# Kernel tuning notes

Hardware: AMD Instinct MI355X
Metric: run time of the kernel (lower is better)

Reference implementation:

```python
import jax, jax.numpy as jnp
import numpy as np

L, H, C = 2, 2, 128            # conv layers, heads, out_channels
N, E, B = 10000, 100000, 64    # nodes, edges, graphs
F_NODE, F_EDGE, FC = 92, 50, 512
HC, C3 = H * C, 3 * C


def _ln(x, g, b, eps=1e-5):
    m = x.mean(-1, keepdims=True)
    v = jnp.var(x, axis=-1, keepdims=True)
    return (x - m) * jax.lax.rsqrt(v + eps) * g + b


def setup_inputs() -> dict:
    key = jax.random.key(0)
    ks = jax.random.split(key, 20)
    r = lambda i, shape, s=0.05: jax.random.normal(ks[i], shape, jnp.float32) * s
    d = {}
    d["x"] = jax.random.normal(ks[0], (N, F_NODE), jnp.float32)
    d["edge_attr"] = jax.random.normal(ks[1], (E, F_EDGE), jnp.float32)
    d["pge"] = jax.random.normal(ks[2], (B, 32), jnp.float32)
    d["cse"] = jax.random.normal(ks[3], (B, 7), jnp.float32)
    d["edge_index"] = jax.random.randint(ks[4], (2, E), 0, N, jnp.int32)
    d["batch"] = jnp.sort(jax.random.randint(ks[5], (N,), 0, B, jnp.int32))
    d["atom_W"] = r(6, (F_NODE, C)); d["atom_b"] = jnp.zeros(C)
    d["edge_W"] = r(7, (F_EDGE, C)); d["edge_b"] = jnp.zeros(C)
    d["Wq"] = r(8, (L, C, HC)); d["bq"] = jnp.zeros((L, HC))
    d["Wk"] = r(9, (L, C, HC)); d["bk"] = jnp.zeros((L, HC))
    d["Wv"] = r(10, (L, C, HC)); d["bv"] = jnp.zeros((L, HC))
    d["We"] = r(11, (L, C, HC))
    d["Wmu"] = r(12, (L, C3, C3)); d["bmu"] = jnp.zeros((L, C3))
    d["Wm"] = r(13, (L, C3, C)); d["bm"] = jnp.zeros((L, C))
    d["ln_m_g"] = jnp.ones((L, C)); d["ln_m_b"] = jnp.zeros((L, C))
    d["ln_a_g"] = jnp.ones((L, C3)); d["ln_a_b"] = jnp.zeros((L, C3))
    d["Wc"] = r(14, (L, HC, C)); d["bc"] = jnp.zeros((L, C))
    d["bn_g"] = jnp.ones((L, C)); d["bn_b"] = jnp.zeros((L, C))
    d["Wskip"] = r(15, (L, C, C)); d["bskip"] = jnp.zeros((L, C))
    d["fc_W"] = r(16, (C + 32 + 7, FC)); d["fc_b"] = jnp.zeros(FC)
    d["out_W"] = r(17, (FC, 1)); d["out_b"] = jnp.zeros(1)
    return d


def reference(x, edge_attr, pge, cse, edge_index, batch, atom_W, atom_b,
              edge_W, edge_b, Wq, bq, Wk, bk, Wv, bv, We, Wmu, bmu, Wm, bm,
              ln_m_g, ln_m_b, ln_a_g, ln_a_b, Wc, bc, bn_g, bn_b, Wskip,
              bskip, fc_W, fc_b, out_W, out_b):
    src, dst = edge_index[0], edge_index[1]  # j = source, i = target
    nf = x @ atom_W + atom_b                 # [N, C]
    ef = edge_attr @ edge_W + edge_b         # [E, C]
    scale = 1.0 / np.sqrt(C3).astype(np.float32)
    for i in range(L):
        q = (nf @ Wq[i] + bq[i]).reshape(N, H, C)
        k = (nf @ Wk[i] + bk[i]).reshape(N, H, C)
        v = (nf @ Wv[i] + bv[i]).reshape(N, H, C)
        ea = (ef @ We[i]).reshape(E, H, C)
        qi = q[dst]
        qcat = jnp.concatenate([qi, qi, qi], -1)                 # [E,H,3C]
        kcat = jnp.concatenate([k[dst], k[src], ea], -1)         # [E,H,3C]
        alpha = qcat * kcat * scale
        gate = jax.nn.sigmoid(_ln(alpha, ln_a_g[i], ln_a_b[i]))
        m = jnp.concatenate([v[dst], v[src], ea], -1)            # [E,H,3C]
        m = (jnp.einsum('ehf,fg->ehg', m, Wmu[i]) + bmu[i]) * gate
        m = jnp.einsum('ehf,fc->ehc', m, Wm[i]) + bm[i]          # [E,H,C]
        m = _ln(m, ln_m_g[i], ln_m_b[i])
        agg = jax.ops.segment_sum(m, dst, num_segments=N)        # scatter-add
        o = agg.reshape(N, HC) @ Wc[i] + bc[i]                   # lin_concate
        mu = o.mean(0); var = jnp.var(o, axis=0)                 # BN (batch stats)
        o = (o - mu) * jax.lax.rsqrt(var + 1e-5) * bn_g[i] + bn_b[i]
        o = jax.nn.silu(o)
        nf = o + nf @ Wskip[i] + bskip[i]                        # root skip
    sums = jax.ops.segment_sum(nf, batch, num_segments=B)
    cnt = jax.ops.segment_sum(jnp.ones((N, 1), nf.dtype), batch, num_segments=B)
    pooled = sums / jnp.maximum(cnt, 1.0)                        # global_mean_pool
    feats = jnp.concatenate([pooled, pge, cse], 1)               # [B, C+39]
    h = jax.nn.silu(feats @ fc_W + fc_b)
    return h @ out_W + out_b                                     # [B, 1]
```

## Files before the change

### kernel.cpp

```cpp
#include <hip/hip_runtime.h>
#include <math.h>

#define N_NODES 10000
#define N_EDGES 100000
#define N_GRAPH 64
#define CDIM 128
#define HCDIM 256
#define C3DIM 384

typedef unsigned short u16;
typedef __attribute__((ext_vector_type(8))) short bf16x8;
typedef __attribute__((ext_vector_type(4))) float f32x4;

__device__ __forceinline__ u16 f2bf(float f) {
  union { float f; unsigned int u; } x; x.f = f;
  unsigned int u = x.u + 0x7fffu + ((x.u >> 16) & 1u);
  return (u16)(u >> 16);
}
__device__ __forceinline__ float bf2f(u16 h) {
  union { unsigned int u; float f; } x; x.u = ((unsigned int)h) << 16;
  return x.f;
}

template<int OUT_BF16, int DO_STATS>
__global__ __launch_bounds__(256) void mfma_gemm_kernel(
    const u16* __restrict__ Ab, const u16* __restrict__ WT,
    const float* __restrict__ bias, void* __restrict__ Y,
    u16* __restrict__ Ymirror, float* __restrict__ cs, float* __restrict__ cs2,
    int M, int K, int N) {
  const int tid = threadIdx.x;
  const int w = tid >> 6, l = tid & 63;
  const int lq = l >> 4, ln = l & 15;
  const int bm = blockIdx.y * 128, bn = blockIdx.x * 64;
  int ra = bm + w * 32 + ln;      if (ra > M - 1) ra = M - 1;
  int rb = bm + w * 32 + 16 + ln; if (rb > M - 1) rb = M - 1;
  f32x4 acc[2][4];
#pragma unroll
  for (int g = 0; g < 2; ++g)
#pragma unroll
    for (int nt = 0; nt < 4; ++nt) acc[g][nt] = {0.f, 0.f, 0.f, 0.f};
  for (int k0 = 0; k0 < K; k0 += 32) {
    bf16x8 a0 = *(const bf16x8*)&Ab[(size_t)ra * K + k0 + lq * 8];
    bf16x8 a1 = *(const bf16x8*)&Ab[(size_t)rb * K + k0 + lq * 8];
#pragma unroll
    for (int nt = 0; nt < 4; ++nt) {
      bf16x8 b = *(const bf16x8*)&WT[(size_t)(bn + nt * 16 + ln) * K + k0 + lq * 8];
      acc[0][nt] = __builtin_amdgcn_mfma_f32_16x16x32_bf16(a0, b, acc[0][nt], 0, 0, 0);
      acc[1][nt] = __builtin_amdgcn_mfma_f32_16x16x32_bf16(a1, b, acc[1][nt], 0, 0, 0);
    }
  }
#pragma unroll
  for (int g = 0; g < 2; ++g) {
    int rowbase = bm + w * 32 + g * 16 + lq * 4;
#pragma unroll
    for (int nt = 0; nt < 4; ++nt) {
      int gn = bn + nt * 16 + ln;
      float bv = bias ? bias[gn] : 0.f;
#pragma unroll
      for (int r = 0; r < 4; ++r) {
        int gm = rowbase + r;
        if (gm < M) {
          float val = acc[g][nt][r] + bv;
          if (OUT_BF16) ((u16*)Y)[(size_t)gm * N + gn] = f2bf(val);
          else          ((float*)Y)[(size_t)gm * N + gn] = val;
          if (Ymirror)  Ymirror[(size_t)gm * N + gn] = f2bf(val);
        }
      }
    }
  }
  if (DO_STATS) {
#pragma unroll
    for (int nt = 0; nt < 4; ++nt) {
      int gn = bn + nt * 16 + ln;
      float bv = bias ? bias[gn] : 0.f;
      float s = 0.f, s2 = 0.f;
#pragma unroll
      for (int g = 0; g < 2; ++g) {
        int rowbase = bm + w * 32 + g * 16 + lq * 4;
#pragma unroll
        for (int r = 0; r < 4; ++r) {
          if (rowbase + r < M) {
            float v = acc[g][nt][r] + bv;
            s += v; s2 += v * v;
          }
        }
      }
      s += __shfl_xor(s, 16); s2 += __shfl_xor(s2, 16);
      s += __shfl_xor(s, 32); s2 += __shfl_xor(s2, 32);
      if (lq == 0) { atomicAdd(&cs[gn], s); atomicAdd(&cs2[gn], s2); }
    }
  }
}

__global__ void pack_init_kernel(
    const float* __restrict__ x, const float* __restrict__ ea,
    const float* __restrict__ atom_W, const float* __restrict__ edge_W,
    u16* __restrict__ xpad, u16* __restrict__ epad,
    u16* __restrict__ atomWT, u16* __restrict__ WeT2) {
  int z = blockIdx.y;
  int idx0 = blockIdx.x * 256 + threadIdx.x;
  const int stride = 256 * 256;
  if (z == 0) {
    for (int idx = idx0; idx < N_NODES * 96; idx += stride) {
      int n = idx / 96, k = idx - n * 96;
      xpad[idx] = (k < 92) ? f2bf(x[(size_t)n * 92 + k]) : (u16)0;
    }
  } else if (z == 1) {
    for (int idx = idx0; idx < N_EDGES * 64; idx += stride) {
      int e = idx >> 6, k = idx & 63;
      epad[idx] = (k < 50) ? f2bf(ea[(size_t)e * 50 + k]) : (u16)0;
    }
  } else if (z == 2) {
    if (idx0 < 128 * 96) { int n = idx0 / 96, k = idx0 - n * 96;
      atomWT[idx0] = (k < 92) ? f2bf(atom_W[(size_t)k * 128 + n]) : (u16)0; }
  } else {
    if (idx0 < 128 * 64) { int n = idx0 >> 6, k = idx0 & 63;
      WeT2[idx0] = (k < 50) ? f2bf(edge_W[(size_t)k * 128 + n]) : (u16)0; }
  }
}

__global__ __launch_bounds__(256) void compose_kernel(
    const float* __restrict__ Wv, const float* __restrict__ We,
    const float* __restrict__ Wmu, u16* __restrict__ WallT,
    u16* __restrict__ WcT) {
  const int z = blockIdx.z;
  const float* Ap; const float* Bp;
  u16* Cp; int colbase;
  if (z < 4) {
    int part = z >> 1, h = z & 1;
    Ap = Wv + h * 128; Bp = Wmu + part * 128 * 384;
    Cp = WallT; colbase = 512 + part * 768 + h * 384;
  } else {
    int h = z - 4;
    Ap = We + h * 128; Bp = Wmu + 256 * 384;
    Cp = WcT; colbase = 256 + h * 384;
  }
  __shared__ float As[16][68];
  __shared__ float Bs[16][65];
  const int tid = threadIdx.x;
  const int bm = blockIdx.y * 64, bn = blockIdx.x * 64;
  const int tx = tid & 15, ty = tid >> 4;
  float acc[4][4] = {};
  for (int k0 = 0; k0 < 128; k0 += 16) {
#pragma unroll
    for (int i = 0; i < 4; ++i) {
      int l = tid + i * 256;
      int kk = l & 15, m = l >> 4;
      As[kk][m] = Ap[(size_t)(bm + m) * 256 + k0 + kk];
    }
#pragma unroll
    for (int i = 0; i < 4; ++i) {
      int l = tid + i * 256;
      int n = l & 63, kk = l >> 6;
      Bs[kk][n] = Bp[(size_t)(k0 + kk) * 384 + bn + n];
    }
    __syncthreads();
#pragma unroll
    for (int kk = 0; kk < 16; ++kk) {
      float a[4], b[4];
#pragma unroll
      for (int i = 0; i < 4; ++i) a[i] = As[kk][ty * 4 + i];
#pragma unroll
      for (int j = 0; j < 4; ++j) b[j] = Bs[kk][tx * 4 + j];
#pragma unroll
      for (int i = 0; i < 4; ++i)
#pragma unroll
        for (int j = 0; j < 4; ++j) acc[i][j] += a[i] * b[j];
    }
    __syncthreads();
  }
#pragma unroll
  for (int i = 0; i < 4; ++i) {
    int gk = bm + ty * 4 + i;
#pragma unroll
    for (int j = 0; j < 4; ++j) {
      int gcol = colbase + bn + tx * 4 + j;
      Cp[(size_t)gcol * 128 + gk] = f2bf(acc[i][j]);
    }
  }
}

__global__ void pack_all_kernel(
    const float* __restrict__ Wq, const float* __restrict__ Wk,
    const float* __restrict__ Wc, const float* __restrict__ Wsk,
    const float* __restrict__ Wm_l, const float* __restrict__ bmu,
    const float* __restrict__ bv_l, const float* __restrict__ Wmu,
    const float* __restrict__ bq_l, const float* __restrict__ bk_l,
    const float* __restrict__ We_l,
    u16* __restrict__ WallT, u16* __restrict__ WcTw, u16* __restrict__ WskT,
    u16* __restrict__ WmTb, float* __restrict__ cbv, float* __restrict__ ball,
    float* __restrict__ agg, float* __restrict__ cs, float* __restrict__ cs2,
    u16* __restrict__ WcT) {
  int z = blockIdx.y;
  int idx = blockIdx.x * 256 + threadIdx.x;
  if (z == 0) {
    if (idx < 32768) { int col = idx >> 7, kk = idx & 127;
      WallT[(size_t)col * 128 + kk] = f2bf(Wq[(size_t)kk * 256 + col]); }
  } else if (z == 1) {
    if (idx < 32768) { int col = idx >> 7, kk = idx & 127;
      WallT[(size_t)(256 + col) * 128 + kk] = f2bf(Wk[(size_t)kk * 256 + col]); }
  } else if (z == 2) {
    if (idx < 32768) { int col = idx >> 8, kk = idx & 255;
      WcTw[(size_t)col * 256 + kk] = f2bf(Wc[(size_t)kk * 128 + col]); }
  } else if (z == 3) {
    if (idx < 16384) { int col = idx >> 7, kk = idx & 127;
      WskT[(size_t)col * 128 + kk] = f2bf(Wsk[(size_t)kk * 128 + col]); }
  } else if (z == 4) {
    if (idx < 49152) { int col = idx / 384, kk = idx - col * 384;
      WmTb[idx] = f2bf(Wm_l[(size_t)kk * 128 + col]); }
  } else if (z == 5) {
    if (idx < 768) {
      int h2 = idx / 384, g = idx - h2 * 384;
      float s = bmu[g];
      for (int d = 0; d < 128; ++d)
        s += bv_l[h2 * 128 + d] * (Wmu[(size_t)d * 384 + g] + Wmu[(size_t)(128 + d) * 384 + g]);
      cbv[idx] = s;
    }
  } else if (z == 6) {
    if (idx < 2048) {
      float v = 0.f;
      if (idx < 256) v = bq_l[idx];
      else if (idx < 512) v = bk_l[idx - 256];
      ball[idx] = v;
    }
  } else if (z == 7) {
    for (int p = idx; p < N_NODES * HCDIM; p += 192 * 256) agg[p] = 0.f;
    if (idx < 128) { cs[idx] = 0.f; cs2[idx] = 0.f; }
  } else {
    if (idx < 32768) { int col = idx >> 7, kk = idx & 127;
      WcT[(size_t)col * 128 + kk] = f2bf(We_l[(size_t)kk * 256 + col]); }
  }
}

__global__ void pack_bf16_kernel(const float* __restrict__ A, u16* __restrict__ B, int n) {
  int idx = blockIdx.x * blockDim.x + threadIdx.x;
  if (idx < n) B[idx] = f2bf(A[idx]);
}

__global__ __launch_bounds__(256, 3) void edge_kernel(
    const u16* __restrict__ qkp, const u16* __restrict__ efb,
    const int* __restrict__ ei, const u16* __restrict__ WcT,
    const float* __restrict__ cbv,
    const float* __restrict__ lag, const float* __restrict__ lab,
    const u16* __restrict__ WmT, const float* __restrict__ bm_l,
    const float* __restrict__ lmg, const float* __restrict__ lmb,
    float* __restrict__ agg, int E) {
  __shared__ __align__(16) u16 C1[16 * 1032];
  __shared__ __align__(16) u16 A2p[12 * 512];
  __shared__ int did16[16];
  float* C2 = (float*)A2p;
  const int tid = threadIdx.x;
  const int e0 = blockIdx.x * 16;
  const int w = tid >> 6, l = tid & 63;
  const int lq = l >> 4, ln = l & 15;
  const float scale = 0.051031036307982884f;

  if (tid < 16) did16[tid] = ei[E + e0 + tid];

  const int r = tid >> 4, lx = tid & 15;
  const int hA = r >> 3, eA = r & 7;

  bf16x8 qv[2], kdv[2], ksv[2], pdv[2][3], psv[2][3];
#pragma unroll
  for (int s = 0; s < 2; ++s) {
    int edge = e0 + s * 8 + eA;
    int dstn = ei[E + edge], srcn = ei[edge];
    const u16* db = qkp + (size_t)dstn * 2048;
    const u16* sb = qkp + (size_t)srcn * 2048;
    qv[s]  = *(const bf16x8*)&db[hA * 128 + lx * 8];
    kdv[s] = *(const bf16x8*)&db[256 + hA * 128 + lx * 8];
    ksv[s] = *(const bf16x8*)&sb[256 + hA * 128 + lx * 8];
#pragma unroll
    for (int p = 0; p < 3; ++p) {
      pdv[s][p] = *(const bf16x8*)&db[512 + hA * 384 + p * 128 + lx * 8];
      psv[s][p] = *(const bf16x8*)&sb[512 + 768 + hA * 384 + p * 128 + lx * 8];
    }
  }

  {
    bf16x8 afr[4];
    const u16* ab = efb + (size_t)(e0 + ln) * 128 + lq * 8;
#pragma unroll
    for (int ks = 0; ks < 4; ++ks) afr[ks] = *(const bf16x8*)(ab + ks * 32);
    for (int nt = 0; nt < 16; ++nt) {
      int g = w * 16 + nt;
      const u16* bb = WcT + (size_t)(g * 16 + ln) * 128 + lq * 8;
      f32x4 acc = {0.f, 0.f, 0.f, 0.f};
#pragma unroll
      for (int ks = 0; ks < 4; ++ks)
        acc = __builtin_amdgcn_mfma_f32_16x16x32_bf16(
            afr[ks], *(const bf16x8*)(bb + ks * 32), acc, 0, 0, 0);
      int col = g * 16 + ln;
#pragma unroll
      for (int rr = 0; rr < 4; ++rr) C1[(lq * 4 + rr) * 1032 + col] = f2bf(acc[rr]);
    }
  }
  __syncthreads();

  for (int s = 0; s < 2; ++s) {
    {
      bf16x8 sea = *(const bf16x8*)&C1[(s * 8 + eA) * 1032 + hA * 128 + lx * 8];
      float a0[8], a1[8], a2[8];
      float sacc = 0.f, s2acc = 0.f;
#pragma unroll
      for (int j = 0; j < 8; ++j) {
        float qf = bf2f((u16)qv[s][j]);
        float x0 = qf * bf2f((u16)kdv[s][j]) * scale;
        float x1 = qf * bf2f((u16)ksv[s][j]) * scale;
        float x2 = qf * bf2f((u16)sea[j]) * scale;
        a0[j] = x0; a1[j] = x1; a2[j] = x2;
        sacc += x0 + x1 + x2;
        s2acc += x0 * x0 + x1 * x1 + x2 * x2;
      }
#pragma unroll
      for (int mm = 1; mm < 16; mm <<= 1) {
        sacc += __shfl_xor(sacc, mm); s2acc += __shfl_xor(s2acc, mm);
      }
      float mean = sacc * (1.f / C3DIM);
      float rstd = rsqrtf(s2acc * (1.f / C3DIM) - mean * mean + 1e-5f);
#pragma unroll
      for (int p = 0; p < 3; ++p) {
        const float* lg = lag + p * 128 + lx * 8;
        const float* lb = lab + p * 128 + lx * 8;
        f32x4 g0 = *(const f32x4*)lg, g1 = *(const f32x4*)(lg + 4);
        f32x4 b0 = *(const f32x4*)lb, b1 = *(const f32x4*)(lb + 4);
        f32x4 c0 = *(const f32x4*)&cbv[hA * 384 + p * 128 + lx * 8];
        f32x4 c1 = *(const f32x4*)&cbv[hA * 384 + p * 128 + lx * 8 + 4];
        bf16x8 pe = *(const bf16x8*)&C1[(s * 8 + eA) * 1032 + 256 + hA * 384 + p * 128 + lx * 8];
        bf16x8 outv;
#pragma unroll
        for (int j = 0; j < 8; ++j) {
          float av = p == 0 ? a0[j] : (p == 1 ? a1[j] : a2[j]);
          float gg = j < 4 ? g0[j] : g1[j - 4];
          float bb2 = j < 4 ? b0[j] : b1[j - 4];
          float cbj = j < 4 ? c0[j] : c1[j - 4];
          float z = (av - mean) * rstd * gg + bb2;
          float gate = 1.f / (1.f + expf(-z));
          float t = (bf2f((u16)pe[j]) + bf2f((u16)pdv[s][p][j]) +
                     bf2f((u16)psv[s][p][j]) + cbj) * gate;
          outv[j] = (short)f2bf(t);
        }
        int ks = p * 4 + (lx >> 2), qq = lx & 3;
        int slot = (((r ^ (qq << 2)) + ks) & 15) | (qq << 4);
        *(bf16x8*)&A2p[ks * 512 + slot * 8] = outv;
      }
    }
    __syncthreads();

    {
      bf16x8 af2[12];
#pragma unroll
      for (int ks = 0; ks < 12; ++ks) {
        int slot = (((ln ^ (lq << 2)) + ks) & 15) | (lq << 4);
        af2[ks] = *(const bf16x8*)&A2p[ks * 512 + slot * 8];
      }
      __syncthreads();
#pragma unroll
      for (int nt = 0; nt < 2; ++nt) {
        int g = w * 2 + nt;
        const u16* bb = WmT + (size_t)(g * 16 + ln) * 384 + lq * 8;
        f32x4 acc = {0.f, 0.f, 0.f, 0.f};
#pragma unroll
        for (int ks = 0; ks < 12; ++ks)
          acc = __builtin_amdgcn_mfma_f32_16x16x32_bf16(
              af2[ks], *(const bf16x8*)(bb + ks * 32), acc, 0, 0, 0);
        int col = g * 16 + ln;
        float bcol = bm_l[col];
#pragma unroll
        for (int rr = 0; rr < 4; ++rr) C2[(lq * 4 + rr) * 132 + col] = acc[rr] + bcol;
      }
    }
    __syncthreads();

    {
      for (int rw = w; rw < 16; rw += 4) {
        float v0 = C2[rw * 132 + l], v1 = C2[rw * 132 + l + 64];
        float sa = v0 + v1, s2a = v0 * v0 + v1 * v1;
#pragma unroll
        for (int off2 = 32; off2 > 0; off2 >>= 1) {
          sa += __shfl_down(sa, off2); s2a += __shfl_down(s2a, off2);
        }
        sa = __shfl(sa, 0); s2a = __shfl(s2a, 0);
        float mean = sa * (1.f / CDIM);
        float rstd = rsqrtf(s2a * (1.f / CDIM) - mean * mean + 1e-5f);
        int h = rw >> 3, e = rw & 7;
        int dstn = did16[s * 8 + e];
        float o0 = (v0 - mean) * rstd * lmg[l] + lmb[l];
        float o1 = (v1 - mean) * rstd * lmg[l + 64] + lmb[l + 64];
        atomicAdd(&agg[(size_t)dstn * HCDIM + h * CDIM + l], o0);
        atomicAdd(&agg[(size_t)dstn * HCDIM + h * CDIM + l + 64], o1);
      }
    }
    __syncthreads();
  }
}

__global__ void bn_silu_skip_kernel(
    const float* __restrict__ o, const float* __restrict__ skip,
    const float* __restrict__ cs, const float* __restrict__ cs2,
    const float* __restrict__ g, const float* __restrict__ b,
    float* __restrict__ nf, u16* __restrict__ nfb) {
  int idx = blockIdx.x * blockDim.x + threadIdx.x;
  if (idx >= N_NODES * CDIM) return;
  int c = idx & (CDIM - 1);
  float m = cs[c] * (1.f / N_NODES);
  float var = cs2[c] * (1.f / N_NODES) - m * m;
  float rstd = rsqrtf(var + 1e-5f);
  float x = (o[idx] - m) * rstd * g[c] + b[c];
  float sig = 1.f / (1.f + expf(-x));
  float val = x * sig + skip[idx];
  nf[idx] = val;
  nfb[idx] = f2bf(val);
}

__global__ __launch_bounds__(256) void poolfeats_kernel(
    const float* __restrict__ nf, const int* __restrict__ batch,
    const float* __restrict__ pge, const float* __restrict__ cse,
    float* __restrict__ feats) {
  const int b = blockIdx.x, tid = threadIdx.x;
  int lo = 0, hi = N_NODES;
  {
    int L = 0, R = N_NODES;
    while (L < R) { int m2 = (L + R) >> 1; if (batch[m2] < b) L = m2 + 1; else R = m2; }
    lo = L;
    L = lo; R = N_NODES;
    while (L < R) { int m2 = (L + R) >> 1; if (batch[m2] <= b) L = m2 + 1; else R = m2; }
    hi = L;
  }
  __shared__ float sacc[2][128];
  const int half = tid >> 7, c = tid & 127;
  float s = 0.f;
  for (int n = lo + half; n < hi; n += 2) s += nf[(size_t)n * CDIM + c];
  sacc[half][c] = s;
  __syncthreads();
  float cntf = fmaxf((float)(hi - lo), 1.f);
  if (tid < 128) feats[b * 167 + tid] = (sacc[0][tid] + sacc[1][tid]) / cntf;
  else if (tid < 160) feats[b * 167 + 128 + (tid - 128)] = pge[b * 32 + (tid - 128)];
  else if (tid < 167) feats[b * 167 + 160 + (tid - 160)] = cse[b * 7 + (tid - 160)];
}

__global__ __launch_bounds__(256) void fcout_kernel(
    const float* __restrict__ feats, const float* __restrict__ fc_W,
    const float* __restrict__ fc_b, const float* __restrict__ ow,
    const float* __restrict__ ob, float* __restrict__ out) {
  const int b = blockIdx.x, tid = threadIdx.x;
  __shared__ float sf[167];
  if (tid < 167) sf[tid] = feats[b * 167 + tid];
  __syncthreads();
  float acc0 = fc_b[tid], acc1 = fc_b[tid + 256];
  for (int k = 0; k < 167; ++k) {
    float fv = sf[k];
    acc0 += fv * fc_W[(size_t)k * 512 + tid];
    acc1 += fv * fc_W[(size_t)k * 512 + tid + 256];
  }
  float h0 = acc0 / (1.f + expf(-acc0));
  float h1 = acc1 / (1.f + expf(-acc1));
  float s = h0 * ow[tid] + h1 * ow[tid + 256];
  __shared__ float red[4];
#pragma unroll
  for (int off = 32; off > 0; off >>= 1) s += __shfl_down(s, off);
  if ((tid & 63) == 0) red[tid >> 6] = s;
  __syncthreads();
  if (tid == 0) out[b] = red[0] + red[1] + red[2] + red[3] + ob[0];
}

extern "C" void kernel_launch(void* const* d_in, const int* in_sizes, int n_in,
                              void* d_out, int out_size, void* d_ws, size_t ws_size,
                              hipStream_t stream) {
  const float* x         = (const float*)d_in[0];
  const float* edge_attr = (const float*)d_in[1];
  const float* pge       = (const float*)d_in[2];
  const float* cse       = (const float*)d_in[3];
  const int*   ei        = (const int*)d_in[4];
  const int*   batch     = (const int*)d_in[5];
  const float* atom_W    = (const float*)d_in[6];
  const float* atom_b    = (const float*)d_in[7];
  const float* edge_W    = (const float*)d_in[8];
  const float* edge_b    = (const float*)d_in[9];
  const float* Wq        = (const float*)d_in[10];
  const float* bq        = (const float*)d_in[11];
  const float* Wk        = (const float*)d_in[12];
  const float* bk        = (const float*)d_in[13];
  const float* Wv        = (const float*)d_in[14];
  const float* bv        = (const float*)d_in[15];
  const float* We        = (const float*)d_in[16];
  const float* Wmu       = (const float*)d_in[17];
  const float* bmu       = (const float*)d_in[18];
  const float* Wm        = (const float*)d_in[19];
  const float* bm        = (const float*)d_in[20];
  const float* ln_m_g    = (const float*)d_in[21];
  const float* ln_m_b    = (const float*)d_in[22];
  const float* ln_a_g    = (const float*)d_in[23];
  const float* ln_a_b    = (const float*)d_in[24];
  const float* Wc        = (const float*)d_in[25];
  const float* bc        = (const float*)d_in[26];
  const float* bn_g      = (const float*)d_in[27];
  const float* bn_b      = (const float*)d_in[28];
  const float* Wskip     = (const float*)d_in[29];
  const float* bskip     = (const float*)d_in[30];
  const float* fc_W      = (const float*)d_in[31];
  const float* fc_b      = (const float*)d_in[32];
  const float* out_W     = (const float*)d_in[33];
  const float* out_b     = (const float*)d_in[34];

  float* ws = (float*)d_ws;
  size_t off = 0;
  float* nf    = ws + off; off += (size_t)N_NODES * CDIM;
  float* agg   = ws + off; off += (size_t)N_NODES * HCDIM;
  float* o     = ws + off; off += (size_t)N_NODES * CDIM;
  float* skip  = ws + off; off += (size_t)N_NODES * CDIM;
  float* cbv   = ws + off; off += 768;
  float* ball  = ws + off; off += 2048;
  float* csum  = ws + off; off += CDIM;
  float* csum2 = ws + off; off += CDIM;
  float* feats = ws + off; off += (size_t)N_GRAPH * 167;
  u16* efb   = (u16*)(ws + off); off += (size_t)N_EDGES * 64;
  u16* WcT   = (u16*)(ws + off); off += 65536;
  u16* WmTb  = (u16*)(ws + off); off += 24576;
  u16* nfb   = (u16*)(ws + off); off += (size_t)N_NODES * 64;
  u16* aggb  = (u16*)(ws + off); off += (size_t)N_NODES * 128;
  u16* qkp   = (u16*)(ws + off); off += (size_t)N_NODES * 1024;
  u16* WallT = (u16*)(ws + off); off += 131072;
  u16* WcTw  = (u16*)(ws + off); off += 16384;
  u16* WskT  = (u16*)(ws + off); off += 8192;
  u16* xpad  = (u16*)(ws + off); off += (size_t)N_NODES * 48;
  u16* epad  = (u16*)(ws + off); off += (size_t)N_EDGES * 32;
  u16* atomWT= (u16*)(ws + off); off += 6144;
  u16* WeT2  = (u16*)(ws + off); off += 4096;

  pack_init_kernel<<<dim3(256, 4), 256, 0, stream>>>(x, edge_attr, atom_W, edge_W,
                                                     xpad, epad, atomWT, WeT2);
  mfma_gemm_kernel<0, 0><<<dim3(2, 79), 256, 0, stream>>>(
      xpad, atomWT, atom_b, nf, nfb, nullptr, nullptr, N_NODES, 96, CDIM);
  mfma_gemm_kernel<1, 0><<<dim3(2, 782), 256, 0, stream>>>(
      epad, WeT2, edge_b, efb, nullptr, nullptr, nullptr, N_EDGES, 64, CDIM);

  for (int i = 0; i < 2; ++i) {
    const float* Wv_i  = Wv + (size_t)i * CDIM * HCDIM;
    const float* We_i  = We + (size_t)i * CDIM * HCDIM;
    const float* Wmu_i = Wmu + (size_t)i * C3DIM * C3DIM;
    compose_kernel<<<dim3(6, 2, 6), 256, 0, stream>>>(Wv_i, We_i, Wmu_i, WallT, WcT);
    pack_all_kernel<<<dim3(192, 9), 256, 0, stream>>>(
        Wq + (size_t)i * CDIM * HCDIM, Wk + (size_t)i * CDIM * HCDIM,
        Wc + (size_t)i * HCDIM * CDIM, Wskip + (size_t)i * CDIM * CDIM,
        Wm + (size_t)i * C3DIM * CDIM, bmu + i * C3DIM, bv + i * HCDIM, Wmu_i,
        bq + i * HCDIM, bk + i * HCDIM, We_i,
        WallT, WcTw, WskT, WmTb, cbv, ball, agg, csum, csum2, WcT);

    mfma_gemm_kernel<1, 0><<<dim3(32, 79), 256, 0, stream>>>(
        nfb, WallT, ball, qkp, nullptr, nullptr, nullptr, N_NODES, CDIM, 2048);

    edge_kernel<<<dim3(N_EDGES / 16), dim3(256), 0, stream>>>(
        qkp, efb, ei, WcT, cbv,
        ln_a_g + i * C3DIM, ln_a_b + i * C3DIM,
        WmTb, bm + i * CDIM,
        ln_m_g + i * CDIM, ln_m_b + i * CDIM, agg, N_EDGES);

    pack_bf16_kernel<<<dim3((N_NODES * 256 + 255) / 256), dim3(256), 0, stream>>>(
        agg, aggb, N_NODES * 256);
    mfma_gemm_kernel<0, 1><<<dim3(2, 79), 256, 0, stream>>>(
        aggb, WcTw, bc + i * CDIM, o, nullptr, csum, csum2, N_NODES, HCDIM, CDIM);
    mfma_gemm_kernel<0, 0><<<dim3(2, 79), 256, 0, stream>>>(
        nfb, WskT, bskip + i * CDIM, skip, nullptr, nullptr, nullptr, N_NODES, CDIM, CDIM);
    bn_silu_skip_kernel<<<dim3((N_NODES * CDIM + 255) / 256), dim3(256), 0, stream>>>(
        o, skip, csum, csum2, bn_g + i * CDIM, bn_b + i * CDIM, nf, nfb);
  }

  poolfeats_kernel<<<dim3(N_GRAPH), 256, 0, stream>>>(nf, batch, pge, cse, feats);
  fcout_kernel<<<dim3(N_GRAPH), 256, 0, stream>>>(feats, fc_W, fc_b, out_W, out_b,
                                                  (float*)d_out);
}
```

Before: 1.245 ms.

## Fold skip GEMM into QKP GEMM, convert agg to bf16 in-GEMM, merge prep kernels

Appends the skip-projection weights as extra columns of the combined node projection GEMM, so the skip output comes out of the same launch and is read from qkp in the BN/SiLU kernel. The separate agg-to-bf16 pack kernel is removed; the Wc GEMM now loads fp32 agg and converts to bf16 in registers. The compose and pack kernels are merged into a single prep launch. This cuts several launches and an fp32-to-bf16 round trip through memory. In exchange the qkp rows get wider, and the skip term is now stored in bf16 instead of fp32, which slightly lowers its precision.

Result: faster. 1.218 ms (-2.2%).

```diff
diff --git a/kernel.cpp b/kernel.cpp
--- a/kernel.cpp
+++ b/kernel.cpp
@@ -7,6 +7,7 @@
 #define CDIM 128
 #define HCDIM 256
 #define C3DIM 384
+#define QKPW 2176
 
 typedef unsigned short u16;
 typedef __attribute__((ext_vector_type(8))) short bf16x8;
@@ -22,9 +23,9 @@
   return x.f;
 }
 
-template<int OUT_BF16, int DO_STATS>
+template<int OUT_BF16, int DO_STATS, int A_F32>
 __global__ __launch_bounds__(256) void mfma_gemm_kernel(
-    const u16* __restrict__ Ab, const u16* __restrict__ WT,
+    const void* __restrict__ Ain, const u16* __restrict__ WT,
     const float* __restrict__ bias, void* __restrict__ Y,
     u16* __restrict__ Ymirror, float* __restrict__ cs, float* __restrict__ cs2,
     int M, int K, int N) {
@@ -40,8 +41,23 @@
 #pragma unroll
     for (int nt = 0; nt < 4; ++nt) acc[g][nt] = {0.f, 0.f, 0.f, 0.f};
   for (int k0 = 0; k0 < K; k0 += 32) {
-    bf16x8 a0 = *(const bf16x8*)&Ab[(size_t)ra * K + k0 + lq * 8];
-    bf16x8 a1 = *(const bf16x8*)&Ab[(size_t)rb * K + k0 + lq * 8];
+    bf16x8 a0, a1;
+    if (A_F32) {
+      const float* Af = (const float*)Ain;
+      f32x4 p0 = *(const f32x4*)&Af[(size_t)ra * K + k0 + lq * 8];
+      f32x4 p1 = *(const f32x4*)&Af[(size_t)ra * K + k0 + lq * 8 + 4];
+      f32x4 p2 = *(const f32x4*)&Af[(size_t)rb * K + k0 + lq * 8];
+      f32x4 p3 = *(const f32x4*)&Af[(size_t)rb * K + k0 + lq * 8 + 4];
+#pragma unroll
+      for (int j = 0; j < 4; ++j) {
+        a0[j] = (short)f2bf(p0[j]); a0[4 + j] = (short)f2bf(p1[j]);
+        a1[j] = (short)f2bf(p2[j]); a1[4 + j] = (short)f2bf(p3[j]);
+      }
+    } else {
+      const u16* Ab = (const u16*)Ain;
+      a0 = *(const bf16x8*)&Ab[(size_t)ra * K + k0 + lq * 8];
+      a1 = *(const bf16x8*)&Ab[(size_t)rb * K + k0 + lq * 8];
+    }
 #pragma unroll
     for (int nt = 0; nt < 4; ++nt) {
       bf16x8 b = *(const bf16x8*)&WT[(size_t)(bn + nt * 16 + ln) * K + k0 + lq * 8];
@@ -119,80 +135,80 @@
   }
 }
 
-__global__ __launch_bounds__(256) void compose_kernel(
-    const float* __restrict__ Wv, const float* __restrict__ We,
-    const float* __restrict__ Wmu, u16* __restrict__ WallT,
-    u16* __restrict__ WcT) {
-  const int z = blockIdx.z;
-  const float* Ap; const float* Bp;
-  u16* Cp; int colbase;
-  if (z < 4) {
-    int part = z >> 1, h = z & 1;
-    Ap = Wv + h * 128; Bp = Wmu + part * 128 * 384;
-    Cp = WallT; colbase = 512 + part * 768 + h * 384;
-  } else {
-    int h = z - 4;
-    Ap = We + h * 128; Bp = Wmu + 256 * 384;
-    Cp = WcT; colbase = 256 + h * 384;
-  }
-  __shared__ float As[16][68];
-  __shared__ float Bs[16][65];
-  const int tid = threadIdx.x;
-  const int bm = blockIdx.y * 64, bn = blockIdx.x * 64;
-  const int tx = tid & 15, ty = tid >> 4;
-  float acc[4][4] = {};
-  for (int k0 = 0; k0 < 128; k0 += 16) {
-#pragma unroll
-    for (int i = 0; i < 4; ++i) {
-      int l = tid + i * 256;
-      int kk = l & 15, m = l >> 4;
-      As[kk][m] = Ap[(size_t)(bm + m) * 256 + k0 + kk];
-    }
-#pragma unroll
-    for (int i = 0; i < 4; ++i) {
-      int l = tid + i * 256;
-      int n = l & 63, kk = l >> 6;
-      Bs[kk][n] = Bp[(size_t)(k0 + kk) * 384 + bn + n];
-    }
-    __syncthreads();
-#pragma unroll
-    for (int kk = 0; kk < 16; ++kk) {
-      float a[4], b[4];
-#pragma unroll
-      for (int i = 0; i < 4; ++i) a[i] = As[kk][ty * 4 + i];
-#pragma unroll
-      for (int j = 0; j < 4; ++j) b[j] = Bs[kk][tx * 4 + j];
-#pragma unroll
-      for (int i = 0; i < 4; ++i)
-#pragma unroll
-        for (int j = 0; j < 4; ++j) acc[i][j] += a[i] * b[j];
-    }
-    __syncthreads();
-  }
-#pragma unroll
-  for (int i = 0; i < 4; ++i) {
-    int gk = bm + ty * 4 + i;
-#pragma unroll
-    for (int j = 0; j < 4; ++j) {
-      int gcol = colbase + bn + tx * 4 + j;
-      Cp[(size_t)gcol * 128 + gk] = f2bf(acc[i][j]);
-    }
-  }
-}
-
-__global__ void pack_all_kernel(
+__global__ __launch_bounds__(256) void prep_kernel(
+    const float* __restrict__ Wv, const float* __restrict__ We_l,
+    const float* __restrict__ Wmu,
     const float* __restrict__ Wq, const float* __restrict__ Wk,
     const float* __restrict__ Wc, const float* __restrict__ Wsk,
     const float* __restrict__ Wm_l, const float* __restrict__ bmu,
-    const float* __restrict__ bv_l, const float* __restrict__ Wmu,
+    const float* __restrict__ bv_l,
     const float* __restrict__ bq_l, const float* __restrict__ bk_l,
-    const float* __restrict__ We_l,
-    u16* __restrict__ WallT, u16* __restrict__ WcTw, u16* __restrict__ WskT,
+    const float* __restrict__ bsk_l,
+    u16* __restrict__ WallT, u16* __restrict__ WcT, u16* __restrict__ WcTw,
     u16* __restrict__ WmTb, float* __restrict__ cbv, float* __restrict__ ball,
-    float* __restrict__ agg, float* __restrict__ cs, float* __restrict__ cs2,
-    u16* __restrict__ WcT) {
-  int z = blockIdx.y;
-  int idx = blockIdx.x * 256 + threadIdx.x;
+    float* __restrict__ agg, float* __restrict__ cs, float* __restrict__ cs2) {
+  __shared__ float As[16][68];
+  __shared__ float Bs[16][65];
+  const int b = blockIdx.x;
+  const int tid = threadIdx.x;
+  if (b < 72) {
+    const int zc = b / 12, rem = b % 12;
+    const int by = rem / 6, bx = rem % 6;
+    const float* Ap; const float* Bp; u16* Cp; int colbase;
+    if (zc < 4) {
+      int part = zc >> 1, h = zc & 1;
+      Ap = Wv + h * 128; Bp = Wmu + part * 128 * 384;
+      Cp = WallT; colbase = 512 + part * 768 + h * 384;
+    } else {
+      int h = zc - 4;
+      Ap = We_l + h * 128; Bp = Wmu + 256 * 384;
+      Cp = WcT; colbase = 256 + h * 384;
+    }
+    const int bm = by * 64, bn = bx * 64;
+    const int tx = tid & 15, ty = tid >> 4;
+    float acc[4][4] = {};
+    for (int k0 = 0; k0 < 128; k0 += 16) {
+#pragma unroll
+      for (int i = 0; i < 4; ++i) {
+        int l = tid + i * 256;
+        int kk = l & 15, m = l >> 4;
+        As[kk][m] = Ap[(size_t)(bm + m) * 256 + k0 + kk];
+      }
+#pragma unroll
+      for (int i = 0; i < 4; ++i) {
+        int l = tid + i * 256;
+        int n = l & 63, kk = l >> 6;
+        Bs[kk][n] = Bp[(size_t)(k0 + kk) * 384 + bn + n];
+      }
+      __syncthreads();
+#pragma unroll
+      for (int kk = 0; kk < 16; ++kk) {
+        float a[4], bb[4];
+#pragma unroll
+        for (int i = 0; i < 4; ++i) a[i] = As[kk][ty * 4 + i];
+#pragma unroll
+        for (int j = 0; j < 4; ++j) bb[j] = Bs[kk][tx * 4 + j];
+#pragma unroll
+        for (int i = 0; i < 4; ++i)
+#pragma unroll
+          for (int j = 0; j < 4; ++j) acc[i][j] += a[i] * bb[j];
+      }
+      __syncthreads();
+    }
+#pragma unroll
+    for (int i = 0; i < 4; ++i) {
+      int gk = bm + ty * 4 + i;
+#pragma unroll
+      for (int j = 0; j < 4; ++j) {
+        int gcol = colbase + bn + tx * 4 + j;
+        Cp[(size_t)gcol * 128 + gk] = f2bf(acc[i][j]);
+      }
+    }
+    return;
+  }
+  const int pb = b - 72;
+  const int z = pb / 192;
+  const int idx = (pb % 192) * 256 + tid;
   if (z == 0) {
     if (idx < 32768) { int col = idx >> 7, kk = idx & 127;
       WallT[(size_t)col * 128 + kk] = f2bf(Wq[(size_t)kk * 256 + col]); }
@@ -204,7 +220,7 @@
       WcTw[(size_t)col * 256 + kk] = f2bf(Wc[(size_t)kk * 128 + col]); }
   } else if (z == 3) {
     if (idx < 16384) { int col = idx >> 7, kk = idx & 127;
-      WskT[(size_t)col * 128 + kk] = f2bf(Wsk[(size_t)kk * 128 + col]); }
+      WallT[(size_t)(2048 + col) * 128 + kk] = f2bf(Wsk[(size_t)kk * 128 + col]); }
   } else if (z == 4) {
     if (idx < 49152) { int col = idx / 384, kk = idx - col * 384;
       WmTb[idx] = f2bf(Wm_l[(size_t)kk * 128 + col]); }
@@ -217,10 +233,11 @@
       cbv[idx] = s;
     }
   } else if (z == 6) {
-    if (idx < 2048) {
+    if (idx < QKPW) {
       float v = 0.f;
       if (idx < 256) v = bq_l[idx];
       else if (idx < 512) v = bk_l[idx - 256];
+      else if (idx >= 2048) v = bsk_l[idx - 2048];
       ball[idx] = v;
     }
   } else if (z == 7) {
@@ -230,11 +247,6 @@
     if (idx < 32768) { int col = idx >> 7, kk = idx & 127;
       WcT[(size_t)col * 128 + kk] = f2bf(We_l[(size_t)kk * 256 + col]); }
   }
-}
-
-__global__ void pack_bf16_kernel(const float* __restrict__ A, u16* __restrict__ B, int n) {
-  int idx = blockIdx.x * blockDim.x + threadIdx.x;
-  if (idx < n) B[idx] = f2bf(A[idx]);
 }
 
 __global__ __launch_bounds__(256, 3) void edge_kernel(
@@ -265,8 +277,8 @@
   for (int s = 0; s < 2; ++s) {
     int edge = e0 + s * 8 + eA;
     int dstn = ei[E + edge], srcn = ei[edge];
-    const u16* db = qkp + (size_t)dstn * 2048;
-    const u16* sb = qkp + (size_t)srcn * 2048;
+    const u16* db = qkp + (size_t)dstn * QKPW;
+    const u16* sb = qkp + (size_t)srcn * QKPW;
     qv[s]  = *(const bf16x8*)&db[hA * 128 + lx * 8];
     kdv[s] = *(const bf16x8*)&db[256 + hA * 128 + lx * 8];
     ksv[s] = *(const bf16x8*)&sb[256 + hA * 128 + lx * 8];
@@ -396,19 +408,21 @@
 }
 
 __global__ void bn_silu_skip_kernel(
-    const float* __restrict__ o, const float* __restrict__ skip,
+    const float* __restrict__ o, const u16* __restrict__ qkp,
     const float* __restrict__ cs, const float* __restrict__ cs2,
     const float* __restrict__ g, const float* __restrict__ b,
     float* __restrict__ nf, u16* __restrict__ nfb) {
   int idx = blockIdx.x * blockDim.x + threadIdx.x;
   if (idx >= N_NODES * CDIM) return;
   int c = idx & (CDIM - 1);
+  int n = idx >> 7;
   float m = cs[c] * (1.f / N_NODES);
   float var = cs2[c] * (1.f / N_NODES) - m * m;
   float rstd = rsqrtf(var + 1e-5f);
   float x = (o[idx] - m) * rstd * g[c] + b[c];
   float sig = 1.f / (1.f + expf(-x));
-  float val = x * sig + skip[idx];
+  float skipv = bf2f(qkp[(size_t)n * QKPW + 2048 + c]);
+  float val = x * sig + skipv;
   nf[idx] = val;
   nfb[idx] = f2bf(val);
 }
@@ -508,9 +522,8 @@
   float* nf    = ws + off; off += (size_t)N_NODES * CDIM;
   float* agg   = ws + off; off += (size_t)N_NODES * HCDIM;
   float* o     = ws + off; off += (size_t)N_NODES * CDIM;
-  float* skip  = ws + off; off += (size_t)N_NODES * CDIM;
   float* cbv   = ws + off; off += 768;
-  float* ball  = ws + off; off += 2048;
+  float* ball  = ws + off; off += QKPW;
   float* csum  = ws + off; off += CDIM;
   float* csum2 = ws + off; off += CDIM;
   float* feats = ws + off; off += (size_t)N_GRAPH * 167;
@@ -518,11 +531,9 @@
   u16* WcT   = (u16*)(ws + off); off += 65536;
   u16* WmTb  = (u16*)(ws + off); off += 24576;
   u16* nfb   = (u16*)(ws + off); off += (size_t)N_NODES * 64;
-  u16* aggb  = (u16*)(ws + off); off += (size_t)N_NODES * 128;
-  u16* qkp   = (u16*)(ws + off); off += (size_t)N_NODES * 1024;
-  u16* WallT = (u16*)(ws + off); off += 131072;
+  u16* qkp   = (u16*)(ws + off); off += (size_t)N_NODES * (QKPW/2);
+  u16* WallT = (u16*)(ws + off); off += (size_t)QKPW * 64;
   u16* WcTw  = (u16*)(ws + off); off += 16384;
-  u16* WskT  = (u16*)(ws + off); off += 8192;
   u16* xpad  = (u16*)(ws + off); off += (size_t)N_NODES * 48;
   u16* epad  = (u16*)(ws + off); off += (size_t)N_EDGES * 32;
   u16* atomWT= (u16*)(ws + off); off += 6144;
@@ -530,25 +541,23 @@
 
   pack_init_kernel<<<dim3(256, 4), 256, 0, stream>>>(x, edge_attr, atom_W, edge_W,
                                                      xpad, epad, atomWT, WeT2);
-  mfma_gemm_kernel<0, 0><<<dim3(2, 79), 256, 0, stream>>>(
+  mfma_gemm_kernel<0, 0, 0><<<dim3(2, 79), 256, 0, stream>>>(
       xpad, atomWT, atom_b, nf, nfb, nullptr, nullptr, N_NODES, 96, CDIM);
-  mfma_gemm_kernel<1, 0><<<dim3(2, 782), 256, 0, stream>>>(
+  mfma_gemm_kernel<1, 0, 0><<<dim3(2, 782), 256, 0, stream>>>(
       epad, WeT2, edge_b, efb, nullptr, nullptr, nullptr, N_EDGES, 64, CDIM);
 
   for (int i = 0; i < 2; ++i) {
-    const float* Wv_i  = Wv + (size_t)i * CDIM * HCDIM;
-    const float* We_i  = We + (size_t)i * CDIM * HCDIM;
-    const float* Wmu_i = Wmu + (size_t)i * C3DIM * C3DIM;
-    compose_kernel<<<dim3(6, 2, 6), 256, 0, stream>>>(Wv_i, We_i, Wmu_i, WallT, WcT);
-    pack_all_kernel<<<dim3(192, 9), 256, 0, stream>>>(
+    prep_kernel<<<dim3(1800), 256, 0, stream>>>(
+        Wv + (size_t)i * CDIM * HCDIM, We + (size_t)i * CDIM * HCDIM,
+        Wmu + (size_t)i * C3DIM * C3DIM,
         Wq + (size_t)i * CDIM * HCDIM, Wk + (size_t)i * CDIM * HCDIM,
         Wc + (size_t)i * HCDIM * CDIM, Wskip + (size_t)i * CDIM * CDIM,
-        Wm + (size_t)i * C3DIM * CDIM, bmu + i * C3DIM, bv + i * HCDIM, Wmu_i,
-        bq + i * HCDIM, bk + i * HCDIM, We_i,
-        WallT, WcTw, WskT, WmTb, cbv, ball, agg, csum, csum2, WcT);
-
-    mfma_gemm_kernel<1, 0><<<dim3(32, 79), 256, 0, stream>>>(
-        nfb, WallT, ball, qkp, nullptr, nullptr, nullptr, N_NODES, CDIM, 2048);
+        Wm + (size_t)i * C3DIM * CDIM, bmu + i * C3DIM, bv + i * HCDIM,
+        bq + i * HCDIM, bk + i * HCDIM, bskip + i * CDIM,
+        WallT, WcT, WcTw, WmTb, cbv, ball, agg, csum, csum2);
+
+    mfma_gemm_kernel<1, 0, 0><<<dim3(QKPW / 64, 79), 256, 0, stream>>>(
+        nfb, WallT, ball, qkp, nullptr, nullptr, nullptr, N_NODES, CDIM, QKPW);
 
     edge_kernel<<<dim3(N_EDGES / 16), dim3(256), 0, stream>>>(
         qkp, efb, ei, WcT, cbv,
@@ -556,14 +565,11 @@
         WmTb, bm + i * CDIM,
         ln_m_g + i * CDIM, ln_m_b + i * CDIM, agg, N_EDGES);
 
-    pack_bf16_kernel<<<dim3((N_NODES * 256 + 255) / 256), dim3(256), 0, stream>>>(
-        agg, aggb, N_NODES * 256);
-    mfma_gemm_kernel<0, 1><<<dim3(2, 79), 256, 0, stream>>>(
-        aggb, WcTw, bc + i * CDIM, o, nullptr, csum, csum2, N_NODES, HCDIM, CDIM);
-    mfma_gemm_kernel<0, 0><<<dim3(2, 79), 256, 0, stream>>>(
-        nfb, WskT, bskip + i * CDIM, skip, nullptr, nullptr, nullptr, N_NODES, CDIM, CDIM);
+    mfma_gemm_kernel<0, 1, 1><<<dim3(2, 79), 256, 0, stream>>>(
+        agg, WcTw, bc + i * CDIM, o, nullptr, csum, csum2, N_NODES, HCDIM, CDIM);
+
     bn_silu_skip_kernel<<<dim3((N_NODES * CDIM + 255) / 256), dim3(256), 0, stream>>>(
-        o, skip, csum, csum2, bn_g + i * CDIM, bn_b + i * CDIM, nf, nfb);
+        o, qkp, csum, csum2, bn_g + i * CDIM, bn_b + i * CDIM, nf, nfb);
   }
 
   poolfeats_kernel<<<dim3(N_GRAPH), 256, 0, stream>>>(nf, batch, pge, cse, feats);
```
